# Kernel tuning notes

Measured on AMD Instinct MI355X. Metric: run time of the kernel, lower is better.

The kernel has to match this reference:

```python
import jax, jax.numpy as jnp
import numpy as np
from jax import lax

B = 8192; LE = 40; LD = 12; PQ = 237; IN = PQ + 19; H = 64


def setup_inputs() -> dict:
    key = jax.random.key(0)
    ks = jax.random.split(key, 26)
    def n(k, shape, s=0.05):
        return jax.random.normal(k, shape, jnp.float32) * s
    return {
        "input_p_q": jax.random.normal(ks[0], (B, LE, PQ), jnp.float32),
        "label_p": jax.random.normal(ks[1], (B, LE), jnp.float32),
        "emb_hour": n(ks[2], (24, 5)),
        "emb_weekday": n(ks[3], (8, 3)),
        "emb_month": n(ks[4], (13, 4)),
        "emb_woy": n(ks[5], (54, 7)),
        "Wi_w": n(ks[6], (H, IN)), "Wi_b": n(ks[7], (H,)),
        "We_w": n(ks[8], (H, 2 * H)),
        "Vd_w": n(ks[9], (IN, H)), "Vd_b": n(ks[10], (IN,)),
        "enc_Wih": n(ks[11], (4 * H, IN)), "enc_Whh": n(ks[12], (4 * H, H)),
        "enc_bih": n(ks[13], (4 * H,)), "enc_bhh": n(ks[14], (4 * H,)),
        "Wd_w": n(ks[15], (H, H)), "Wd_b": n(ks[16], (H,)),
        "Wd2_w": n(ks[17], (H, 2)),
        "Vdt_w": n(ks[18], (1, H)), "Vdt_b": n(ks[19], (1,)),
        "dec_Wih": n(ks[20], (4, H + 1)), "dec_Whh": n(ks[21], (4, 1)),
        "dec_bih": n(ks[22], (4,)), "dec_bhh": n(ks[23], (4,)),
        "input_time": jax.random.randint(ks[24], (B, LE, 4), 0, 8),
        "decoder_time": jax.random.randint(ks[25], (B, LD), 0, 24),
    }


def _lstm_cell(x, h, c, Wih, Whh, bih, bhh):
    # PyTorch LSTMCell gate order: i, f, g, o
    g = x @ Wih.T + bih + h @ Whh.T + bhh
    i, f, gg, o = jnp.split(g, 4, axis=1)
    c = jax.nn.sigmoid(f) * c + jax.nn.sigmoid(i) * jnp.tanh(gg)
    h = jax.nn.sigmoid(o) * jnp.tanh(c)
    return h, c


def _forward(input_p_q, label_p, emb_hour, emb_weekday, emb_month, emb_woy,
             Wi_w, Wi_b, We_w, Vd_w, Vd_b,
             enc_Wih, enc_Whh, enc_bih, enc_bhh,
             Wd_w, Wd_b, Wd2_w, Vdt_w, Vdt_b,
             dec_Wih, dec_Whh, dec_bih, dec_bhh, input_time):
    b = input_p_q.shape[0]
    inputs = jnp.concatenate([
        input_p_q,
        emb_hour[input_time[:, :, 0]],
        emb_weekday[input_time[:, :, 1]],
        emb_month[input_time[:, :, 2]],
        emb_woy[input_time[:, :, 3]],
    ], axis=2)  # [B, LE, IN]

    def enc_step(carry, x_t):
        h, c = carry
        score = jnp.tanh(jnp.concatenate([h, c], 1) @ We_w.T
                         + x_t @ Wi_w.T + Wi_b) @ Vd_w.T + Vd_b  # [B, IN]
        x_in = x_t * jax.nn.softmax(score, axis=1)
        h, c = _lstm_cell(x_in, h, c, enc_Wih, enc_Whh, enc_bih, enc_bhh)
        return (h, c), h

    z = jnp.zeros((b, H), inputs.dtype)
    _, mid = lax.scan(enc_step, (z, z), jnp.swapaxes(inputs, 0, 1))
    mid_output = jnp.swapaxes(mid, 0, 1)  # [B, LE, H]

    wd_mid = mid_output @ Wd_w.T + Wd_b  # precompute Wd(mid_output), [B, LE, H]
    dec_p_in = label_p[:, LE - 1:LE]  # [B, 1], held constant across decode steps

    def dec_step(carry, _):
        hi, ci = carry  # [B, 1] each
        q = jnp.concatenate([hi, ci], 1) @ Wd2_w.T  # [B, H]
        score = jnp.tanh(q[:, None, :] + wd_mid) @ Vdt_w.T + Vdt_b  # [B, LE, 1] (no softmax, as in source)
        ctx = jnp.einsum('bt,btd->bd', score[..., 0], mid_output)  # [B, H]
        hi, ci = _lstm_cell(jnp.concatenate([ctx, dec_p_in], 1), hi, ci,
                            dec_Wih, dec_Whh, dec_bih, dec_bhh)
        return (hi, ci), hi

    z1 = jnp.zeros((b, 1), inputs.dtype)
    _, outs = lax.scan(dec_step, (z1, z1), None, length=LD)  # [LD, B, 1]
    return jnp.swapaxes(outs[..., 0], 0, 1)  # [B, LD]


def reference(input_p_q, label_p, emb_hour, emb_weekday, emb_month, emb_woy,
              Wi_w, Wi_b, We_w, Vd_w, Vd_b,
              enc_Wih, enc_Whh, enc_bih, enc_bhh,
              Wd_w, Wd_b, Wd2_w, Vdt_w, Vdt_b,
              dec_Wih, dec_Whh, dec_bih, dec_bhh, input_time, decoder_time):
    # decoder_time is accepted by the original forward but never used
    return _forward(input_p_q, label_p, emb_hour, emb_weekday, emb_month, emb_woy,
                    Wi_w, Wi_b, We_w, Vd_w, Vd_b,
                    enc_Wih, enc_Whh, enc_bih, enc_bhh,
                    Wd_w, Wd_b, Wd2_w, Vdt_w, Vdt_b,
                    dec_Wih, dec_Whh, dec_bih, dec_bhh, input_time)
```

## Files before the change

### kernel.cpp

```cpp
#include <hip/hip_runtime.h>

#define BB   8192
#define LEN  40
#define LDN  12
#define PQN  237
#define INN  256
#define HN   64
#define BT   32
#define ENC_BLOCKS (BB / BT)
#define DW   8
#define DEC_BLOCKS (BB / DW)
#define XPS  256

typedef unsigned int  u32;
typedef _Float16 f16;
typedef f16  half8 __attribute__((ext_vector_type(8)));
typedef f16  f16x4 __attribute__((ext_vector_type(4)));
typedef float f32x4 __attribute__((ext_vector_type(4)));

#define XS 264
#define HS 72

#define OFF_WI   0
#define OFF_WE   16384
#define OFF_VD   24576
#define OFF_WIH  40960
#define OFF_WHH  106496
#define OFF_WD   122880
#define W_TOTAL  126976

#define T_H   0
#define T_W   120
#define T_M   144
#define T_Y   196
#define T_TOT 574

__device__ __forceinline__ float rcp_(float x){
#if __has_builtin(__builtin_amdgcn_rcpf)
  return __builtin_amdgcn_rcpf(x);
#else
  return 1.0f / x;
#endif
}
__device__ __forceinline__ float sigm(float x){
  return rcp_(1.0f + exp2f(-1.44269504f * x));
}
__device__ __forceinline__ float tanhf_(float x){
  x = fminf(15.0f, fmaxf(-15.0f, x));
  float e = exp2f(2.88539008f * x);
  return (e - 1.0f) * rcp_(e + 1.0f);
}

__device__ __forceinline__ void bar_lds(){
  asm volatile("s_waitcnt lgkmcnt(0)" ::: "memory");
  __builtin_amdgcn_s_barrier();
  asm volatile("" ::: "memory");
}

__global__ __launch_bounds__(256) void conv_w(
    const float* __restrict__ Wi, const float* __restrict__ We,
    const float* __restrict__ Vd, const float* __restrict__ Wih,
    const float* __restrict__ Whh, const float* __restrict__ Wd,
    f16* __restrict__ dst)
{
  int i = blockIdx.x * 256 + threadIdx.x;
  if (i >= W_TOTAL) return;
  float v;
  if      (i < OFF_WE)  v = Wi [i - OFF_WI ];
  else if (i < OFF_VD)  v = We [i - OFF_WE ];
  else if (i < OFF_WIH) v = Vd [i - OFF_VD ];
  else if (i < OFF_WHH) v = Wih[i - OFF_WIH];
  else if (i < OFF_WD)  v = Whh[i - OFF_WHH];
  else                  v = Wd [i - OFF_WD ];
  dst[i] = (f16)v;
}

__global__ __launch_bounds__(256) void prep_x(
    const float* __restrict__ ipq,
    const float* __restrict__ e_h, const float* __restrict__ e_w,
    const float* __restrict__ e_m, const float* __restrict__ e_y,
    const int*  __restrict__ itime,
    f16* __restrict__ xpre)
{
  const int wv = threadIdx.x >> 6, l = threadIdx.x & 63;
  const size_t row0 = (size_t)blockIdx.x * 32 + (size_t)wv * 8;
  for (int r = 0; r < 8; ++r) {
    const size_t row = row0 + r;
    const float* src = ipq + row * PQN;
    const int*  it   = itime + row * 4;
    f16* dst = xpre + row * XPS;
    #pragma unroll
    for (int k = 0; k < 4; ++k) {
      const int c = k * 64 + l;
      float v;
      if (c < PQN) v = src[c];
      else {
        const int o = c - PQN;
        if      (o < 5 ) v = e_h[it[0] * 5 + o];
        else if (o < 8 ) v = e_w[it[1] * 3 + (o - 5)];
        else if (o < 12) v = e_m[it[2] * 4 + (o - 8)];
        else             v = e_y[it[3] * 7 + (o - 12)];
      }
      dst[c] = (f16)v;
    }
  }
}

__global__ __launch_bounds__(256, 1) void enc_x(
    const f16* __restrict__ xpre,
    const float* __restrict__ Wi_b,
    const float* __restrict__ Vd_b,
    const float* __restrict__ ebih, const float* __restrict__ ebhh,
    const float* __restrict__ Wd_b,
    const f16*  __restrict__ wAll,
    f16* __restrict__ xout)
{
  __shared__ __attribute__((aligned(16))) f16 Xl[BT * XS];
  __shared__ __attribute__((aligned(16))) f16 Ul[BT * HS];
  __shared__ __attribute__((aligned(16))) f16 Hl[BT * HS];
  __shared__ __attribute__((aligned(16))) f16 Cl[BT * HS];
  __shared__ float Sred[2 * 64];

  const int tid  = threadIdx.x;
  const int w    = tid >> 6;
  const int lane = tid & 63;
  const int nl   = lane & 15;
  const int q    = lane >> 4;
  const int b0   = blockIdx.x * BT;
  const int d0   = w * 16 + q * 4;

  const int r0  = tid >> 5;
  const int off = tid & 31;
  const f16* gb = xpre + ((size_t)(b0 + r0) * LEN) * XPS + off * 8;
  const u32 lw0 = (u32)(r0 * XS + off * 8);

  half8 sr[4];
  #pragma unroll
  for (int j = 0; j < 4; ++j)
    sr[j] = *(const half8*)(gb + (size_t)(8 * j) * LEN * XPS);

  half8 wif[8], wef[4], vdf[4][2], whf[4][8], whhf[4][2], wdf[2];
  {
    const f16* pw = wAll + OFF_WI + (w * 16 + nl) * 256 + q * 8;
    #pragma unroll
    for (int kt = 0; kt < 8; ++kt) wif[kt] = *(const half8*)(pw + kt * 32);
    const f16* pe = wAll + OFF_WE + (w * 16 + nl) * 128 + q * 8;
    #pragma unroll
    for (int kt = 0; kt < 4; ++kt) wef[kt] = *(const half8*)(pe + kt * 32);
    #pragma unroll
    for (int i = 0; i < 4; ++i) {
      const f16* pv = wAll + OFF_VD + ((w + 4*i) * 16 + nl) * 64 + q * 8;
      #pragma unroll
      for (int kt = 0; kt < 2; ++kt) vdf[i][kt] = *(const half8*)(pv + kt * 32);
      const f16* ph = wAll + OFF_WIH + ((w + 4*i) * 16 + nl) * 256 + q * 8;
      #pragma unroll
      for (int kt = 0; kt < 8; ++kt) whf[i][kt] = *(const half8*)(ph + kt * 32);
      const f16* pq = wAll + OFF_WHH + ((w + 4*i) * 16 + nl) * 64 + q * 8;
      #pragma unroll
      for (int kt = 0; kt < 2; ++kt) whhf[i][kt] = *(const half8*)(pq + kt * 32);
    }
    const f16* pd = wAll + OFF_WD + (w * 16 + nl) * 64 + q * 8;
    #pragma unroll
    for (int kt = 0; kt < 2; ++kt) wdf[kt] = *(const half8*)(pd + kt * 32);
  }

  float wib[4], vdb[16], ebs[16], wdb[4];
  #pragma unroll
  for (int r = 0; r < 4; ++r) { wib[r] = Wi_b[d0 + r]; wdb[r] = Wd_b[d0 + r]; }
  #pragma unroll
  for (int i = 0; i < 4; ++i)
    #pragma unroll
    for (int r = 0; r < 4; ++r) {
      vdb[i*4+r] = Vd_b[(w + 4*i) * 16 + q * 4 + r];
      ebs[i*4+r] = ebih[i * 64 + d0 + r] + ebhh[i * 64 + d0 + r];
    }

  for (int i = tid; i < BT * HS; i += 256) { Hl[i] = (f16)0.f; Cl[i] = (f16)0.f; }
  float creg[2][4];
  #pragma unroll
  for (int bt = 0; bt < 2; ++bt)
    #pragma unroll
    for (int r = 0; r < 4; ++r) creg[bt][r] = 0.f;
  bar_lds();

  for (int t = 0; t < LEN; ++t) {
    #pragma unroll
    for (int j = 0; j < 4; ++j)
      *(half8*)(&Xl[lw0 + j * 8 * XS]) = sr[j];
    if (t + 1 < LEN) {
      const f16* gp = gb + (size_t)(t + 1) * XPS;
      #pragma unroll
      for (int j = 0; j < 4; ++j)
        sr[j] = *(const half8*)(gp + (size_t)(8 * j) * LEN * XPS);
    }
    bar_lds();

    #pragma unroll
    for (int bt = 0; bt < 2; ++bt) {
      const int row = bt * 16 + nl;
      f32x4 acc = {0.f, 0.f, 0.f, 0.f};
      const f16* xb = &Xl[row * XS + q * 8];
      #pragma unroll
      for (int kt = 0; kt < 8; ++kt)
        acc = __builtin_amdgcn_mfma_f32_16x16x32_f16(wif[kt], *(const half8*)(xb + kt * 32), acc, 0, 0, 0);
      const f16* hb = &Hl[row * HS + q * 8];
      const f16* cb = &Cl[row * HS + q * 8];
      half8 h0 = *(const half8*)hb, h1 = *(const half8*)(hb + 32);
      half8 c0 = *(const half8*)cb, c1 = *(const half8*)(cb + 32);
      acc = __builtin_amdgcn_mfma_f32_16x16x32_f16(wef[0], h0, acc, 0, 0, 0);
      acc = __builtin_amdgcn_mfma_f32_16x16x32_f16(wef[1], h1, acc, 0, 0, 0);
      acc = __builtin_amdgcn_mfma_f32_16x16x32_f16(wef[2], c0, acc, 0, 0, 0);
      acc = __builtin_amdgcn_mfma_f32_16x16x32_f16(wef[3], c1, acc, 0, 0, 0);
      f16x4 uv;
      #pragma unroll
      for (int r = 0; r < 4; ++r) uv[r] = (f16)tanhf_(acc[r] + wib[r]);
      *(f16x4*)(&Ul[row * HS + d0]) = uv;
      if (t > 0) {
        f32x4 aw = {0.f, 0.f, 0.f, 0.f};
        aw = __builtin_amdgcn_mfma_f32_16x16x32_f16(wdf[0], h0, aw, 0, 0, 0);
        aw = __builtin_amdgcn_mfma_f32_16x16x32_f16(wdf[1], h1, aw, 0, 0, 0);
        f16x4 wv;
        #pragma unroll
        for (int r = 0; r < 4; ++r) wv[r] = (f16)(aw[r] + wdb[r]);
        *(f16x4*)(&xout[((size_t)(b0 + row) * LEN + (t - 1)) * XPS + 64 + d0]) = wv;
      }
    }
    bar_lds();

    #pragma unroll
    for (int bt = 0; bt < 2; ++bt) {
      const int row = bt * 16 + nl;
      const f16* ub = &Ul[row * HS + q * 8];
      half8 u0 = *(const half8*)ub, u1 = *(const half8*)(ub + 32);
      float ee[16];
      #pragma unroll
      for (int i = 0; i < 4; ++i) {
        f32x4 acc = {0.f, 0.f, 0.f, 0.f};
        acc = __builtin_amdgcn_mfma_f32_16x16x32_f16(vdf[i][0], u0, acc, 0, 0, 0);
        acc = __builtin_amdgcn_mfma_f32_16x16x32_f16(vdf[i][1], u1, acc, 0, 0, 0);
        #pragma unroll
        for (int r = 0; r < 4; ++r)
          ee[i*4+r] = exp2f((acc[r] + vdb[i*4+r]) * 1.44269504f);
      }
      float s = 0.f;
      #pragma unroll
      for (int j = 0; j < 16; ++j) s += ee[j];
      s += __shfl_xor(s, 16, 64);
      s += __shfl_xor(s, 32, 64);
      if (lane < 16) Sred[bt * 64 + w * 16 + lane] = s;
      #pragma unroll
      for (int i = 0; i < 4; ++i) {
        const int k = (w + 4*i) * 16 + q * 4;
        f16x4 xv = *(const f16x4*)(&Xl[row * XS + k]);
        f16x4 pv;
        #pragma unroll
        for (int r = 0; r < 4; ++r) pv[r] = (f16)((float)xv[r] * ee[i*4+r]);
        *(f16x4*)(&Xl[row * XS + k]) = pv;
      }
    }
    bar_lds();

    f16x4 hstash[2], cstash[2];
    #pragma unroll
    for (int bt = 0; bt < 2; ++bt) {
      const int row = bt * 16 + nl;
      f32x4 g[4], gh[4];
      #pragma unroll
      for (int i = 0; i < 4; ++i) {
        g[i]  = (f32x4){0.f, 0.f, 0.f, 0.f};
        gh[i] = (f32x4){0.f, 0.f, 0.f, 0.f};
      }
      const f16* pb = &Xl[row * XS + q * 8];
      #pragma unroll
      for (int kt = 0; kt < 8; ++kt) {
        half8 bv = *(const half8*)(pb + kt * 32);
        #pragma unroll
        for (int i = 0; i < 4; ++i)
          g[i] = __builtin_amdgcn_mfma_f32_16x16x32_f16(whf[i][kt], bv, g[i], 0, 0, 0);
      }
      const f16* hb = &Hl[row * HS + q * 8];
      half8 h0 = *(const half8*)hb, h1 = *(const half8*)(hb + 32);
      #pragma unroll
      for (int i = 0; i < 4; ++i) {
        gh[i] = __builtin_amdgcn_mfma_f32_16x16x32_f16(whhf[i][0], h0, gh[i], 0, 0, 0);
        gh[i] = __builtin_amdgcn_mfma_f32_16x16x32_f16(whhf[i][1], h1, gh[i], 0, 0, 0);
      }
      const float inv = rcp_(Sred[bt*64 + nl]      + Sred[bt*64 + 16 + nl]
                           + Sred[bt*64 + 32 + nl] + Sred[bt*64 + 48 + nl]);
      f16x4 hv, cv;
      #pragma unroll
      for (int r = 0; r < 4; ++r) {
        const float gi = g[0][r] * inv + gh[0][r] + ebs[0  + r];
        const float gf = g[1][r] * inv + gh[1][r] + ebs[4  + r];
        const float gg = g[2][r] * inv + gh[2][r] + ebs[8  + r];
        const float go = g[3][r] * inv + gh[3][r] + ebs[12 + r];
        float c = sigm(gf) * creg[bt][r] + sigm(gi) * tanhf_(gg);
        creg[bt][r] = c;
        const float h = sigm(go) * tanhf_(c);
        hv[r] = (f16)h; cv[r] = (f16)c;
      }
      hstash[bt] = hv; cstash[bt] = cv;
      *(f16x4*)(&xout[((size_t)(b0 + row) * LEN + t) * XPS + d0]) = hv;
    }
    bar_lds();
    #pragma unroll
    for (int bt = 0; bt < 2; ++bt) {
      const int row = bt * 16 + nl;
      *(f16x4*)(&Hl[row * HS + d0]) = hstash[bt];
      *(f16x4*)(&Cl[row * HS + d0]) = cstash[bt];
    }
  }

  bar_lds();
  #pragma unroll
  for (int bt = 0; bt < 2; ++bt) {
    const int row = bt * 16 + nl;
    const f16* hb = &Hl[row * HS + q * 8];
    half8 h0 = *(const half8*)hb, h1 = *(const half8*)(hb + 32);
    f32x4 aw = {0.f, 0.f, 0.f, 0.f};
    aw = __builtin_amdgcn_mfma_f32_16x16x32_f16(wdf[0], h0, aw, 0, 0, 0);
    aw = __builtin_amdgcn_mfma_f32_16x16x32_f16(wdf[1], h1, aw, 0, 0, 0);
    f16x4 wv;
    #pragma unroll
    for (int r = 0; r < 4; ++r) wv[r] = (f16)(aw[r] + wdb[r]);
    *(f16x4*)(&xout[((size_t)(b0 + row) * LEN + (LEN - 1)) * XPS + 64 + d0]) = wv;
  }
}

__global__ __launch_bounds__(256, 1) void enc_fb(
    const float* __restrict__ ipq,
    const float* __restrict__ e_h, const float* __restrict__ e_w,
    const float* __restrict__ e_m, const float* __restrict__ e_y,
    const float* __restrict__ Wi_b, const float* __restrict__ Vd_b,
    const float* __restrict__ ebih, const float* __restrict__ ebhh,
    const float* __restrict__ Wd_b, const f16* __restrict__ wAll,
    const int*  __restrict__ itime,
    f16* __restrict__ mid, f16* __restrict__ wmid)
{
  __shared__ __attribute__((aligned(16))) f16 Xl[BT * XS];
  __shared__ __attribute__((aligned(16))) f16 Ul[BT * HS];
  __shared__ __attribute__((aligned(16))) f16 Hl[BT * HS];
  __shared__ __attribute__((aligned(16))) f16 Cl[BT * HS];
  __shared__ float Sred[2 * 64];
  __shared__ float Tl[T_TOT];

  const int tid  = threadIdx.x;
  const int w    = tid >> 6;
  const int lane = tid & 63;
  const int nl   = lane & 15;
  const int q    = lane >> 4;
  const int b0   = blockIdx.x * BT;
  const int d0   = w * 16 + q * 4;

  const u32* pptr;
  int pstr, tstr, tbase = 0, twid = 0, tsub = 0;
  if (tid < PQN) {
    pptr = (const u32*)ipq + tid; pstr = LEN * PQN; tstr = PQN;
  } else {
    const int o = tid - PQN; int sel;
    if      (o < 5 ) { sel = 0; tbase = T_H; twid = 5; tsub = o;      }
    else if (o < 8 ) { sel = 1; tbase = T_W; twid = 3; tsub = o - 5;  }
    else if (o < 12) { sel = 2; tbase = T_M; twid = 4; tsub = o - 8;  }
    else             { sel = 3; tbase = T_Y; twid = 7; tsub = o - 12; }
    pptr = (const u32*)itime + sel; pstr = LEN * 4; tstr = 4;
  }
  pptr += (size_t)b0 * pstr;

  u32 pf[BT];
  #pragma unroll
  for (int bb = 0; bb < BT; ++bb) pf[bb] = pptr[(size_t)bb * pstr];

  half8 wif[8], wef[4], vdf[4][2], whf[4][8], whhf[4][2], wdf[2];
  {
    const f16* pw = wAll + OFF_WI + (w * 16 + nl) * 256 + q * 8;
    #pragma unroll
    for (int kt = 0; kt < 8; ++kt) wif[kt] = *(const half8*)(pw + kt * 32);
    const f16* pe = wAll + OFF_WE + (w * 16 + nl) * 128 + q * 8;
    #pragma unroll
    for (int kt = 0; kt < 4; ++kt) wef[kt] = *(const half8*)(pe + kt * 32);
    #pragma unroll
    for (int i = 0; i < 4; ++i) {
      const f16* pv = wAll + OFF_VD + ((w + 4*i) * 16 + nl) * 64 + q * 8;
      #pragma unroll
      for (int kt = 0; kt < 2; ++kt) vdf[i][kt] = *(const half8*)(pv + kt * 32);
      const f16* ph = wAll + OFF_WIH + ((w + 4*i) * 16 + nl) * 256 + q * 8;
      #pragma unroll
      for (int kt = 0; kt < 8; ++kt) whf[i][kt] = *(const half8*)(ph + kt * 32);
      const f16* pq = wAll + OFF_WHH + ((w + 4*i) * 16 + nl) * 64 + q * 8;
      #pragma unroll
      for (int kt = 0; kt < 2; ++kt) whhf[i][kt] = *(const half8*)(pq + kt * 32);
    }
    const f16* pd = wAll + OFF_WD + (w * 16 + nl) * 64 + q * 8;
    #pragma unroll
    for (int kt = 0; kt < 2; ++kt) wdf[kt] = *(const half8*)(pd + kt * 32);
  }

  float wib[4], vdb[16], ebs[16], wdb[4];
  #pragma unroll
  for (int r = 0; r < 4; ++r) { wib[r] = Wi_b[d0 + r]; wdb[r] = Wd_b[d0 + r]; }
  #pragma unroll
  for (int i = 0; i < 4; ++i)
    #pragma unroll
    for (int r = 0; r < 4; ++r) {
      vdb[i*4+r] = Vd_b[(w + 4*i) * 16 + q * 4 + r];
      ebs[i*4+r] = ebih[i * 64 + d0 + r] + ebhh[i * 64 + d0 + r];
    }

  for (int i = tid; i < BT * HS; i += 256) { Hl[i] = (f16)0.f; Cl[i] = (f16)0.f; }
  for (int i = tid; i < T_TOT; i += 256) {
    float v;
    if      (i < T_W) v = e_h[i];
    else if (i < T_M) v = e_w[i - T_W];
    else if (i < T_Y) v = e_m[i - T_M];
    else              v = e_y[i - T_Y];
    Tl[i] = v;
  }
  float creg[2][4];
  #pragma unroll
  for (int bt = 0; bt < 2; ++bt)
    #pragma unroll
    for (int r = 0; r < 4; ++r) creg[bt][r] = 0.f;
  bar_lds();

  for (int t = 0; t < LEN; ++t) {
    #pragma unroll
    for (int bb = 0; bb < BT; ++bb) {
      float v;
      if (tid < PQN) v = __uint_as_float(pf[bb]);
      else           v = Tl[tbase + (int)pf[bb] * twid + tsub];
      Xl[bb * XS + tid] = (f16)v;
    }
    if (t + 1 < LEN) {
      const u32* pp = pptr + (size_t)(t + 1) * tstr;
      #pragma unroll
      for (int bb = 0; bb < BT; ++bb) pf[bb] = pp[(size_t)bb * pstr];
    }
    bar_lds();

    #pragma unroll
    for (int bt = 0; bt < 2; ++bt) {
      const int row = bt * 16 + nl;
      f32x4 acc = {0.f, 0.f, 0.f, 0.f};
      const f16* xb = &Xl[row * XS + q * 8];
      #pragma unroll
      for (int kt = 0; kt < 8; ++kt)
        acc = __builtin_amdgcn_mfma_f32_16x16x32_f16(wif[kt], *(const half8*)(xb + kt * 32), acc, 0, 0, 0);
      const f16* hb = &Hl[row * HS + q * 8];
      const f16* cb = &Cl[row * HS + q * 8];
      half8 h0 = *(const half8*)hb, h1 = *(const half8*)(hb + 32);
      half8 c0 = *(const half8*)cb, c1 = *(const half8*)(cb + 32);
      acc = __builtin_amdgcn_mfma_f32_16x16x32_f16(wef[0], h0, acc, 0, 0, 0);
      acc = __builtin_amdgcn_mfma_f32_16x16x32_f16(wef[1], h1, acc, 0, 0, 0);
      acc = __builtin_amdgcn_mfma_f32_16x16x32_f16(wef[2], c0, acc, 0, 0, 0);
      acc = __builtin_amdgcn_mfma_f32_16x16x32_f16(wef[3], c1, acc, 0, 0, 0);
      f16x4 uv;
      #pragma unroll
      for (int r = 0; r < 4; ++r) uv[r] = (f16)tanhf_(acc[r] + wib[r]);
      *(f16x4*)(&Ul[row * HS + d0]) = uv;
      if (t > 0) {
        f32x4 aw = {0.f, 0.f, 0.f, 0.f};
        aw = __builtin_amdgcn_mfma_f32_16x16x32_f16(wdf[0], h0, aw, 0, 0, 0);
        aw = __builtin_amdgcn_mfma_f32_16x16x32_f16(wdf[1], h1, aw, 0, 0, 0);
        f16x4 wv;
        #pragma unroll
        for (int r = 0; r < 4; ++r) wv[r] = (f16)(aw[r] + wdb[r]);
        *(f16x4*)(&wmid[((size_t)(b0 + row) * LEN + (t - 1)) * HN + d0]) = wv;
      }
    }
    bar_lds();

    #pragma unroll
    for (int bt = 0; bt < 2; ++bt) {
      const int row = bt * 16 + nl;
      const f16* ub = &Ul[row * HS + q * 8];
      half8 u0 = *(const half8*)ub, u1 = *(const half8*)(ub + 32);
      float ee[16];
      #pragma unroll
      for (int i = 0; i < 4; ++i) {
        f32x4 acc = {0.f, 0.f, 0.f, 0.f};
        acc = __builtin_amdgcn_mfma_f32_16x16x32_f16(vdf[i][0], u0, acc, 0, 0, 0);
        acc = __builtin_amdgcn_mfma_f32_16x16x32_f16(vdf[i][1], u1, acc, 0, 0, 0);
        #pragma unroll
        for (int r = 0; r < 4; ++r)
          ee[i*4+r] = exp2f((acc[r] + vdb[i*4+r]) * 1.44269504f);
      }
      float s = 0.f;
      #pragma unroll
      for (int j = 0; j < 16; ++j) s += ee[j];
      s += __shfl_xor(s, 16, 64);
      s += __shfl_xor(s, 32, 64);
      if (lane < 16) Sred[bt * 64 + w * 16 + lane] = s;
      #pragma unroll
      for (int i = 0; i < 4; ++i) {
        const int k = (w + 4*i) * 16 + q * 4;
        f16x4 xv = *(const f16x4*)(&Xl[row * XS + k]);
        f16x4 pv;
        #pragma unroll
        for (int r = 0; r < 4; ++r) pv[r] = (f16)((float)xv[r] * ee[i*4+r]);
        *(f16x4*)(&Xl[row * XS + k]) = pv;
      }
    }
    bar_lds();

    f16x4 hstash[2], cstash[2];
    #pragma unroll
    for (int bt = 0; bt < 2; ++bt) {
      const int row = bt * 16 + nl;
      f32x4 g[4], gh[4];
      #pragma unroll
      for (int i = 0; i < 4; ++i) {
        g[i]  = (f32x4){0.f, 0.f, 0.f, 0.f};
        gh[i] = (f32x4){0.f, 0.f, 0.f, 0.f};
      }
      const f16* pb = &Xl[row * XS + q * 8];
      #pragma unroll
      for (int kt = 0; kt < 8; ++kt) {
        half8 bv = *(const half8*)(pb + kt * 32);
        #pragma unroll
        for (int i = 0; i < 4; ++i)
          g[i] = __builtin_amdgcn_mfma_f32_16x16x32_f16(whf[i][kt], bv, g[i], 0, 0, 0);
      }
      const f16* hb = &Hl[row * HS + q * 8];
      half8 h0 = *(const half8*)hb, h1 = *(const half8*)(hb + 32);
      #pragma unroll
      for (int i = 0; i < 4; ++i) {
        gh[i] = __builtin_amdgcn_mfma_f32_16x16x32_f16(whhf[i][0], h0, gh[i], 0, 0, 0);
        gh[i] = __builtin_amdgcn_mfma_f32_16x16x32_f16(whhf[i][1], h1, gh[i], 0, 0, 0);
      }
      const float inv = rcp_(Sred[bt*64 + nl]      + Sred[bt*64 + 16 + nl]
                           + Sred[bt*64 + 32 + nl] + Sred[bt*64 + 48 + nl]);
      f16x4 hv, cv;
      #pragma unroll
      for (int r = 0; r < 4; ++r) {
        const float gi = g[0][r] * inv + gh[0][r] + ebs[0  + r];
        const float gf = g[1][r] * inv + gh[1][r] + ebs[4  + r];
        const float gg = g[2][r] * inv + gh[2][r] + ebs[8  + r];
        const float go = g[3][r] * inv + gh[3][r] + ebs[12 + r];
        float c = sigm(gf) * creg[bt][r] + sigm(gi) * tanhf_(gg);
        creg[bt][r] = c;
        const float h = sigm(go) * tanhf_(c);
        hv[r] = (f16)h; cv[r] = (f16)c;
      }
      hstash[bt] = hv; cstash[bt] = cv;
      *(f16x4*)(&mid[((size_t)(b0 + row) * LEN + t) * HN + d0]) = hv;
    }
    bar_lds();
    #pragma unroll
    for (int bt = 0; bt < 2; ++bt) {
      const int row = bt * 16 + nl;
      *(f16x4*)(&Hl[row * HS + d0]) = hstash[bt];
      *(f16x4*)(&Cl[row * HS + d0]) = cstash[bt];
    }
  }

  bar_lds();
  #pragma unroll
  for (int bt = 0; bt < 2; ++bt) {
    const int row = bt * 16 + nl;
    const f16* hb = &Hl[row * HS + q * 8];
    half8 h0 = *(const half8*)hb, h1 = *(const half8*)(hb + 32);
    f32x4 aw = {0.f, 0.f, 0.f, 0.f};
    aw = __builtin_amdgcn_mfma_f32_16x16x32_f16(wdf[0], h0, aw, 0, 0, 0);
    aw = __builtin_amdgcn_mfma_f32_16x16x32_f16(wdf[1], h1, aw, 0, 0, 0);
    f16x4 wv;
    #pragma unroll
    for (int r = 0; r < 4; ++r) wv[r] = (f16)(aw[r] + wdb[r]);
    *(f16x4*)(&wmid[((size_t)(b0 + row) * LEN + (LEN - 1)) * HN + d0]) = wv;
  }
}

#define WMS 56

__global__ __launch_bounds__(512) void dec_kernel(
    const f16* __restrict__ mids,
    const f16* __restrict__ wms,
    const int MS,
    const float* __restrict__ lblp,
    const float* __restrict__ Wd2_w,
    const float* __restrict__ Vdt_w,
    const float* __restrict__ Vdt_b,
    const float* __restrict__ dWih,
    const float* __restrict__ dWhh,
    const float* __restrict__ dbih, const float* __restrict__ dbhh,
    float* __restrict__ out)
{
  __shared__ __attribute__((aligned(16))) f16  wml[DW][LEN * WMS];
  __shared__ __attribute__((aligned(16))) float qv[DW][HN];
  __shared__ __attribute__((aligned(16))) float vs[HN];
  __shared__ __attribute__((aligned(16))) float ws4[4 * 65];

  const int w    = threadIdx.x >> 6;
  const int lane = threadIdx.x & 63;
  const int b    = blockIdx.x * DW + w;

  for (int t = 0; t < LEN; ++t)
    wml[w][t * WMS + lane] = wms[((size_t)b * LEN + t) * MS + lane];
  if (threadIdx.x < HN)      vs[threadIdx.x]  = Vdt_w[threadIdx.x];
  if (threadIdx.x < 4 * 65)  ws4[threadIdx.x] = dWih[threadIdx.x];
  __syncthreads();

  float macc[4] = {0.f, 0.f, 0.f, 0.f};
  if (lane < LEN) {
    const f16* mrow = mids + ((size_t)b * LEN + lane) * MS;
    #pragma unroll
    for (int k8 = 0; k8 < 8; ++k8) {
      half8 mv = *(const half8*)(mrow + k8 * 8);
      #pragma unroll
      for (int e = 0; e < 8; ++e) {
        const float m = (float)mv[e];
        #pragma unroll
        for (int j = 0; j < 4; ++j) macc[j] += ws4[j * 65 + k8 * 8 + e] * m;
      }
    }
  }

  const float dpin = lblp[b * LEN + (LEN - 1)];
  const float w20 = Wd2_w[2 * lane];
  const float w21 = Wd2_w[2 * lane + 1];
  const float vdtb = Vdt_b[0];
  float wxx[4], whh4[4], bb4[4];
  #pragma unroll
  for (int j = 0; j < 4; ++j) {
    wxx[j]  = dWih[j * 65 + 64];
    whh4[j] = dWhh[j];
    bb4[j]  = dbih[j] + dbhh[j];
  }

  float hi = 0.0f, ci = 0.0f;
  for (int s = 0; s < LDN; ++s) {
    qv[w][lane] = w20 * hi + w21 * ci;

    float p0 = 0.f, p1 = 0.f, p2 = 0.f, p3 = 0.f;
    if (lane < LEN) {
      const f16* wrow = &wml[w][lane * WMS];
      float acc = 0.f;
      #pragma unroll
      for (int k8 = 0; k8 < 8; ++k8) {
        float4 qa = *(const float4*)&qv[w][k8 * 8];
        float4 qb = *(const float4*)&qv[w][k8 * 8 + 4];
        float4 va = *(const float4*)&vs[k8 * 8];
        float4 vb = *(const float4*)&vs[k8 * 8 + 4];
        half8 wv = *(const half8*)(wrow + k8 * 8);
        acc += tanhf_(qa.x + (float)wv[0]) * va.x
             + tanhf_(qa.y + (float)wv[1]) * va.y
             + tanhf_(qa.z + (float)wv[2]) * va.z
             + tanhf_(qa.w + (float)wv[3]) * va.w
             + tanhf_(qb.x + (float)wv[4]) * vb.x
             + tanhf_(qb.y + (float)wv[5]) * vb.y
             + tanhf_(qb.z + (float)wv[6]) * vb.z
             + tanhf_(qb.w + (float)wv[7]) * vb.w;
      }
      const float score = acc + vdtb;
      p0 = score * macc[0]; p1 = score * macc[1];
      p2 = score * macc[2]; p3 = score * macc[3];
    }
    #pragma unroll
    for (int off = 32; off >= 1; off >>= 1) {
      p0 += __shfl_xor(p0, off, 64);
      p1 += __shfl_xor(p1, off, 64);
      p2 += __shfl_xor(p2, off, 64);
      p3 += __shfl_xor(p3, off, 64);
    }
    const float g0 = p0 + wxx[0] * dpin + bb4[0] + whh4[0] * hi;
    const float g1 = p1 + wxx[1] * dpin + bb4[1] + whh4[1] * hi;
    const float g2 = p2 + wxx[2] * dpin + bb4[2] + whh4[2] * hi;
    const float g3 = p3 + wxx[3] * dpin + bb4[3] + whh4[3] * hi;
    ci = sigm(g1) * ci + sigm(g0) * tanhf_(g2);
    hi = sigm(g3) * tanhf_(ci);
    if (lane == 0) out[b * LDN + s] = hi;
  }
}

extern "C" void kernel_launch(void* const* d_in, const int* in_sizes, int n_in,
                              void* d_out, int out_size, void* d_ws, size_t ws_size,
                              hipStream_t stream) {
  (void)in_sizes; (void)n_in; (void)out_size;
  const float* ipq   = (const float*)d_in[0];
  const float* lblp  = (const float*)d_in[1];
  const float* e_h   = (const float*)d_in[2];
  const float* e_w   = (const float*)d_in[3];
  const float* e_m   = (const float*)d_in[4];
  const float* e_y   = (const float*)d_in[5];
  const float* Wi_w  = (const float*)d_in[6];
  const float* Wi_b  = (const float*)d_in[7];
  const float* We_w  = (const float*)d_in[8];
  const float* Vd_w  = (const float*)d_in[9];
  const float* Vd_b  = (const float*)d_in[10];
  const float* eWih  = (const float*)d_in[11];
  const float* eWhh  = (const float*)d_in[12];
  const float* ebih  = (const float*)d_in[13];
  const float* ebhh  = (const float*)d_in[14];
  const float* Wd_w  = (const float*)d_in[15];
  const float* Wd_b  = (const float*)d_in[16];
  const float* Wd2_w = (const float*)d_in[17];
  const float* Vdt_w = (const float*)d_in[18];
  const float* Vdt_b = (const float*)d_in[19];
  const float* dWih  = (const float*)d_in[20];
  const float* dWhh  = (const float*)d_in[21];
  const float* dbih  = (const float*)d_in[22];
  const float* dbhh  = (const float*)d_in[23];
  const int* itime   = (const int*)d_in[24];
  float* out = (float*)d_out;

  const size_t xpreB = (size_t)BB * LEN * XPS * 2;
  const size_t wcvtB = (size_t)W_TOTAL * 2;

  if (ws_size >= xpreB + wcvtB) {
    f16* xpre = (f16*)d_ws;
    f16* wcvt = (f16*)((char*)d_ws + xpreB);
    conv_w<<<dim3((W_TOTAL + 255) / 256), dim3(256), 0, stream>>>(
        Wi_w, We_w, Vd_w, eWih, eWhh, Wd_w, wcvt);
    prep_x<<<dim3(BB * LEN / 32), dim3(256), 0, stream>>>(
        ipq, e_h, e_w, e_m, e_y, itime, xpre);
    enc_x<<<dim3(ENC_BLOCKS), dim3(256), 0, stream>>>(
        xpre, Wi_b, Vd_b, ebih, ebhh, Wd_b, wcvt, xpre);
    dec_kernel<<<dim3(DEC_BLOCKS), dim3(512), 0, stream>>>(
        xpre, xpre + 64, XPS, lblp, Wd2_w, Vdt_w, Vdt_b,
        dWih, dWhh, dbih, dbhh, out);
  } else {
    const size_t midB = (size_t)BB * LEN * HN * 2;
    f16* mid  = (f16*)d_ws;
    f16* wmid = (f16*)((char*)d_ws + midB);
    f16* wcvt = (f16*)((char*)d_ws + 2 * midB);
    conv_w<<<dim3((W_TOTAL + 255) / 256), dim3(256), 0, stream>>>(
        Wi_w, We_w, Vd_w, eWih, eWhh, Wd_w, wcvt);
    enc_fb<<<dim3(ENC_BLOCKS), dim3(256), 0, stream>>>(
        ipq, e_h, e_w, e_m, e_y, Wi_b, Vd_b, ebih, ebhh, Wd_b, wcvt, itime,
        mid, wmid);
    dec_kernel<<<dim3(DEC_BLOCKS), dim3(512), 0, stream>>>(
        mid, wmid, HN, lblp, Wd2_w, Vdt_w, Vdt_b,
        dWih, dWhh, dbih, dbhh, out);
  }
}
```

Before: 939.0 us.

## Double-buffer encoder LDS, coalesce outputs, merge prep kernels, register decoder rows

```diff
diff --git a/kernel.cpp b/kernel.cpp
--- a/kernel.cpp
+++ b/kernel.cpp
@@ -35,6 +35,9 @@
 #define T_Y   196
 #define T_TOT 574
 
+#define PREP_BLOCKS (BB * LEN / 32)
+#define CONV_BLOCKS ((W_TOTAL + 255) / 256)
+
 __device__ __forceinline__ float rcp_(float x){
 #if __has_builtin(__builtin_amdgcn_rcpf)
   return __builtin_amdgcn_rcpf(x);
@@ -46,9 +49,8 @@
   return rcp_(1.0f + exp2f(-1.44269504f * x));
 }
 __device__ __forceinline__ float tanhf_(float x){
-  x = fminf(15.0f, fmaxf(-15.0f, x));
   float e = exp2f(2.88539008f * x);
-  return (e - 1.0f) * rcp_(e + 1.0f);
+  return 1.0f - 2.0f * rcp_(e + 1.0f);
 }
 
 __device__ __forceinline__ void bar_lds(){
@@ -75,31 +77,56 @@
   dst[i] = (f16)v;
 }
 
-__global__ __launch_bounds__(256) void prep_x(
+__global__ __launch_bounds__(256) void prep_all(
     const float* __restrict__ ipq,
     const float* __restrict__ e_h, const float* __restrict__ e_w,
     const float* __restrict__ e_m, const float* __restrict__ e_y,
     const int*  __restrict__ itime,
-    f16* __restrict__ xpre)
+    f16* __restrict__ xpre,
+    const float* __restrict__ Wi, const float* __restrict__ We,
+    const float* __restrict__ Vd, const float* __restrict__ Wih,
+    const float* __restrict__ Whh, const float* __restrict__ Wd,
+    f16* __restrict__ wdst)
 {
+  if (blockIdx.x >= PREP_BLOCKS) {
+    int i = (blockIdx.x - PREP_BLOCKS) * 256 + threadIdx.x;
+    if (i >= W_TOTAL) return;
+    float v;
+    if      (i < OFF_WE)  v = Wi [i - OFF_WI ];
+    else if (i < OFF_VD)  v = We [i - OFF_WE ];
+    else if (i < OFF_WIH) v = Vd [i - OFF_VD ];
+    else if (i < OFF_WHH) v = Wih[i - OFF_WIH];
+    else if (i < OFF_WD)  v = Whh[i - OFF_WHH];
+    else                  v = Wd [i - OFF_WD ];
+    wdst[i] = (f16)v;
+    return;
+  }
   const int wv = threadIdx.x >> 6, l = threadIdx.x & 63;
   const size_t row0 = (size_t)blockIdx.x * 32 + (size_t)wv * 8;
+  int4 itv[8];
+  #pragma unroll
+  for (int r = 0; r < 8; ++r)
+    itv[r] = *(const int4*)(itime + (row0 + r) * 4);
+  #pragma unroll
   for (int r = 0; r < 8; ++r) {
     const size_t row = row0 + r;
     const float* src = ipq + row * PQN;
-    const int*  it   = itime + row * 4;
     f16* dst = xpre + row * XPS;
     #pragma unroll
-    for (int k = 0; k < 4; ++k) {
+    for (int k = 0; k < 3; ++k) {
       const int c = k * 64 + l;
+      dst[c] = (f16)src[c];
+    }
+    {
+      const int c = 192 + l;
       float v;
       if (c < PQN) v = src[c];
       else {
         const int o = c - PQN;
-        if      (o < 5 ) v = e_h[it[0] * 5 + o];
-        else if (o < 8 ) v = e_w[it[1] * 3 + (o - 5)];
-        else if (o < 12) v = e_m[it[2] * 4 + (o - 8)];
-        else             v = e_y[it[3] * 7 + (o - 12)];
+        if      (o < 5 ) v = e_h[itv[r].x * 5 + o];
+        else if (o < 8 ) v = e_w[itv[r].y * 3 + (o - 5)];
+        else if (o < 12) v = e_m[itv[r].z * 4 + (o - 8)];
+        else             v = e_y[itv[r].w * 7 + (o - 12)];
       }
       dst[c] = (f16)v;
     }
@@ -115,10 +142,11 @@
     const f16*  __restrict__ wAll,
     f16* __restrict__ xout)
 {
-  __shared__ __attribute__((aligned(16))) f16 Xl[BT * XS];
+  __shared__ __attribute__((aligned(16))) f16 Xl[2][BT * XS];
   __shared__ __attribute__((aligned(16))) f16 Ul[BT * HS];
-  __shared__ __attribute__((aligned(16))) f16 Hl[BT * HS];
-  __shared__ __attribute__((aligned(16))) f16 Cl[BT * HS];
+  __shared__ __attribute__((aligned(16))) f16 Hl[2][BT * HS];
+  __shared__ __attribute__((aligned(16))) f16 Cl[2][BT * HS];
+  __shared__ __attribute__((aligned(16))) f16 Wml[BT * HS];
   __shared__ float Sred[2 * 64];
 
   const int tid  = threadIdx.x;
@@ -134,6 +162,9 @@
   const f16* gb = xpre + ((size_t)(b0 + r0) * LEN) * XPS + off * 8;
   const u32 lw0 = (u32)(r0 * XS + off * 8);
 
+  const int orow = tid >> 3;
+  const int oc8  = (tid & 7) * 8;
+
   half8 sr[4];
   #pragma unroll
   for (int j = 0; j < 4; ++j)
@@ -175,7 +206,9 @@
       ebs[i*4+r] = ebih[i * 64 + d0 + r] + ebhh[i * 64 + d0 + r];
     }
 
-  for (int i = tid; i < BT * HS; i += 256) { Hl[i] = (f16)0.f; Cl[i] = (f16)0.f; }
+  for (int i = tid; i < BT * HS; i += 256) {
+    Hl[0][i] = (f16)0.f; Cl[0][i] = (f16)0.f;
+  }
   float creg[2][4];
   #pragma unroll
   for (int bt = 0; bt < 2; ++bt)
@@ -184,9 +217,10 @@
   bar_lds();
 
   for (int t = 0; t < LEN; ++t) {
+    const int cur = t & 1, nxt = cur ^ 1;
     #pragma unroll
     for (int j = 0; j < 4; ++j)
-      *(half8*)(&Xl[lw0 + j * 8 * XS]) = sr[j];
+      *(half8*)(&Xl[cur][lw0 + j * 8 * XS]) = sr[j];
     if (t + 1 < LEN) {
       const f16* gp = gb + (size_t)(t + 1) * XPS;
       #pragma unroll
@@ -199,12 +233,12 @@
     for (int bt = 0; bt < 2; ++bt) {
       const int row = bt * 16 + nl;
       f32x4 acc = {0.f, 0.f, 0.f, 0.f};
-      const f16* xb = &Xl[row * XS + q * 8];
+      const f16* xb = &Xl[cur][row * XS + q * 8];
       #pragma unroll
       for (int kt = 0; kt < 8; ++kt)
         acc = __builtin_amdgcn_mfma_f32_16x16x32_f16(wif[kt], *(const half8*)(xb + kt * 32), acc, 0, 0, 0);
-      const f16* hb = &Hl[row * HS + q * 8];
-      const f16* cb = &Cl[row * HS + q * 8];
+      const f16* hb = &Hl[cur][row * HS + q * 8];
+      const f16* cb = &Cl[cur][row * HS + q * 8];
       half8 h0 = *(const half8*)hb, h1 = *(const half8*)(hb + 32);
       half8 c0 = *(const half8*)cb, c1 = *(const half8*)(cb + 32);
       acc = __builtin_amdgcn_mfma_f32_16x16x32_f16(wef[0], h0, acc, 0, 0, 0);
@@ -222,11 +256,18 @@
         f16x4 wv;
         #pragma unroll
         for (int r = 0; r < 4; ++r) wv[r] = (f16)(aw[r] + wdb[r]);
-        *(f16x4*)(&xout[((size_t)(b0 + row) * LEN + (t - 1)) * XPS + 64 + d0]) = wv;
+        *(f16x4*)(&Wml[row * HS + d0]) = wv;
       }
     }
     bar_lds();
 
+    if (t > 0) {
+      half8 hv8 = *(const half8*)(&Hl[cur][orow * HS + oc8]);
+      half8 wv8 = *(const half8*)(&Wml[orow * HS + oc8]);
+      f16* xr = xout + ((size_t)(b0 + orow) * LEN + (t - 1)) * XPS;
+      *(half8*)(xr + oc8)      = hv8;
+      *(half8*)(xr + 64 + oc8) = wv8;
+    }
     #pragma unroll
     for (int bt = 0; bt < 2; ++bt) {
       const int row = bt * 16 + nl;
@@ -251,16 +292,15 @@
       #pragma unroll
       for (int i = 0; i < 4; ++i) {
         const int k = (w + 4*i) * 16 + q * 4;
-        f16x4 xv = *(const f16x4*)(&Xl[row * XS + k]);
+        f16x4 xv = *(const f16x4*)(&Xl[cur][row * XS + k]);
         f16x4 pv;
         #pragma unroll
         for (int r = 0; r < 4; ++r) pv[r] = (f16)((float)xv[r] * ee[i*4+r]);
-        *(f16x4*)(&Xl[row * XS + k]) = pv;
+        *(f16x4*)(&Xl[cur][row * XS + k]) = pv;
       }
     }
     bar_lds();
 
-    f16x4 hstash[2], cstash[2];
     #pragma unroll
     for (int bt = 0; bt < 2; ++bt) {
       const int row = bt * 16 + nl;
@@ -270,7 +310,7 @@
         g[i]  = (f32x4){0.f, 0.f, 0.f, 0.f};
         gh[i] = (f32x4){0.f, 0.f, 0.f, 0.f};
       }
-      const f16* pb = &Xl[row * XS + q * 8];
+      const f16* pb = &Xl[cur][row * XS + q * 8];
       #pragma unroll
       for (int kt = 0; kt < 8; ++kt) {
         half8 bv = *(const half8*)(pb + kt * 32);
@@ -278,7 +318,7 @@
         for (int i = 0; i < 4; ++i)
           g[i] = __builtin_amdgcn_mfma_f32_16x16x32_f16(whf[i][kt], bv, g[i], 0, 0, 0);
       }
-      const f16* hb = &Hl[row * HS + q * 8];
+      const f16* hb = &Hl[cur][row * HS + q * 8];
       half8 h0 = *(const half8*)hb, h1 = *(const half8*)(hb + 32);
       #pragma unroll
       for (int i = 0; i < 4; ++i) {
@@ -299,15 +339,8 @@
         const float h = sigm(go) * tanhf_(c);
         hv[r] = (f16)h; cv[r] = (f16)c;
       }
-      hstash[bt] = hv; cstash[bt] = cv;
-      *(f16x4*)(&xout[((size_t)(b0 + row) * LEN + t) * XPS + d0]) = hv;
-    }
-    bar_lds();
-    #pragma unroll
-    for (int bt = 0; bt < 2; ++bt) {
-      const int row = bt * 16 + nl;
-      *(f16x4*)(&Hl[row * HS + d0]) = hstash[bt];
-      *(f16x4*)(&Cl[row * HS + d0]) = cstash[bt];
+      *(f16x4*)(&Hl[nxt][row * HS + d0]) = hv;
+      *(f16x4*)(&Cl[nxt][row * HS + d0]) = cv;
     }
   }
 
@@ -315,7 +348,7 @@
   #pragma unroll
   for (int bt = 0; bt < 2; ++bt) {
     const int row = bt * 16 + nl;
-    const f16* hb = &Hl[row * HS + q * 8];
+    const f16* hb = &Hl[0][row * HS + q * 8];
     half8 h0 = *(const half8*)hb, h1 = *(const half8*)(hb + 32);
     f32x4 aw = {0.f, 0.f, 0.f, 0.f};
     aw = __builtin_amdgcn_mfma_f32_16x16x32_f16(wdf[0], h0, aw, 0, 0, 0);
@@ -323,7 +356,15 @@
     f16x4 wv;
     #pragma unroll
     for (int r = 0; r < 4; ++r) wv[r] = (f16)(aw[r] + wdb[r]);
-    *(f16x4*)(&xout[((size_t)(b0 + row) * LEN + (LEN - 1)) * XPS + 64 + d0]) = wv;
+    *(f16x4*)(&Wml[row * HS + d0]) = wv;
+  }
+  bar_lds();
+  {
+    half8 hv8 = *(const half8*)(&Hl[0][orow * HS + oc8]);
+    half8 wv8 = *(const half8*)(&Wml[orow * HS + oc8]);
+    f16* xr = xout + ((size_t)(b0 + orow) * LEN + (LEN - 1)) * XPS;
+    *(half8*)(xr + oc8)      = hv8;
+    *(half8*)(xr + 64 + oc8) = wv8;
   }
 }
 
@@ -569,8 +610,6 @@
   }
 }
 
-#define WMS 56
-
 __global__ __launch_bounds__(512) void dec_kernel(
     const f16* __restrict__ mids,
     const f16* __restrict__ wms,
@@ -584,7 +623,6 @@
     const float* __restrict__ dbih, const float* __restrict__ dbhh,
     float* __restrict__ out)
 {
-  __shared__ __attribute__((aligned(16))) f16  wml[DW][LEN * WMS];
   __shared__ __attribute__((aligned(16))) float qv[DW][HN];
   __shared__ __attribute__((aligned(16))) float vs[HN];
   __shared__ __attribute__((aligned(16))) float ws4[4 * 65];
@@ -593,10 +631,20 @@
   const int lane = threadIdx.x & 63;
   const int b    = blockIdx.x * DW + w;
 
-  for (int t = 0; t < LEN; ++t)
-    wml[w][t * WMS + lane] = wms[((size_t)b * LEN + t) * MS + lane];
-  if (threadIdx.x < HN)      vs[threadIdx.x]  = Vdt_w[threadIdx.x];
-  if (threadIdx.x < 4 * 65)  ws4[threadIdx.x] = dWih[threadIdx.x];
+  if (threadIdx.x < HN)     vs[threadIdx.x]  = Vdt_w[threadIdx.x];
+  if (threadIdx.x < 4 * 65) ws4[threadIdx.x] = dWih[threadIdx.x];
+
+  half8 wmr[8];
+  if (lane < LEN) {
+    const f16* p = wms + ((size_t)b * LEN + lane) * MS;
+    #pragma unroll
+    for (int k = 0; k < 8; ++k) wmr[k] = *(const half8*)(p + k * 8);
+  } else {
+    #pragma unroll
+    for (int k = 0; k < 8; ++k)
+      #pragma unroll
+      for (int e = 0; e < 8; ++e) wmr[k][e] = (f16)0.f;
+  }
   __syncthreads();
 
   float macc[4] = {0.f, 0.f, 0.f, 0.f};
@@ -632,7 +680,6 @@
 
     float p0 = 0.f, p1 = 0.f, p2 = 0.f, p3 = 0.f;
     if (lane < LEN) {
-      const f16* wrow = &wml[w][lane * WMS];
       float acc = 0.f;
       #pragma unroll
       for (int k8 = 0; k8 < 8; ++k8) {
@@ -640,7 +687,7 @@
         float4 qb = *(const float4*)&qv[w][k8 * 8 + 4];
         float4 va = *(const float4*)&vs[k8 * 8];
         float4 vb = *(const float4*)&vs[k8 * 8 + 4];
-        half8 wv = *(const half8*)(wrow + k8 * 8);
+        half8 wv = wmr[k8];
         acc += tanhf_(qa.x + (float)wv[0]) * va.x
              + tanhf_(qa.y + (float)wv[1]) * va.y
              + tanhf_(qa.z + (float)wv[2]) * va.z
@@ -708,10 +755,9 @@
   if (ws_size >= xpreB + wcvtB) {
     f16* xpre = (f16*)d_ws;
     f16* wcvt = (f16*)((char*)d_ws + xpreB);
-    conv_w<<<dim3((W_TOTAL + 255) / 256), dim3(256), 0, stream>>>(
+    prep_all<<<dim3(PREP_BLOCKS + CONV_BLOCKS), dim3(256), 0, stream>>>(
+        ipq, e_h, e_w, e_m, e_y, itime, xpre,
         Wi_w, We_w, Vd_w, eWih, eWhh, Wd_w, wcvt);
-    prep_x<<<dim3(BB * LEN / 32), dim3(256), 0, stream>>>(
-        ipq, e_h, e_w, e_m, e_y, itime, xpre);
     enc_x<<<dim3(ENC_BLOCKS), dim3(256), 0, stream>>>(
         xpre, Wi_b, Vd_b, ebih, ebhh, Wd_b, wcvt, xpre);
     dec_kernel<<<dim3(DEC_BLOCKS), dim3(512), 0, stream>>>(
@@ -722,7 +768,7 @@
     f16* mid  = (f16*)d_ws;
     f16* wmid = (f16*)((char*)d_ws + midB);
     f16* wcvt = (f16*)((char*)d_ws + 2 * midB);
-    conv_w<<<dim3((W_TOTAL + 255) / 256), dim3(256), 0, stream>>>(
+    conv_w<<<dim3(CONV_BLOCKS), dim3(256), 0, stream>>>(
         Wi_w, We_w, Vd_w, eWih, eWhh, Wd_w, wcvt);
     enc_fb<<<dim3(ENC_BLOCKS), dim3(256), 0, stream>>>(
         ipq, e_h, e_w, e_m, e_y, Wi_b, Vd_b, ebih, ebhh, Wd_b, wcvt, itime,
```

Result: faster. 876.3 us (-6.7%).
